# Performance work log

Hardware: AMD Instinct MI355X
Metric: run time of the kernel (lower is better)

The kernel has to match this reference:

```python
import jax, jax.numpy as jnp
import numpy as np

N_NODES = 50000
N_EDGES = 800000
IN_DIM = 128
OUT_DIM = 256


def setup_inputs() -> dict:
    key = jax.random.key(0)
    k1, k2, k3, k4 = jax.random.split(key, 4)
    feat = jax.random.normal(k1, (N_NODES, IN_DIM), dtype=jnp.float32)
    # xavier_uniform with relu gain, shape [in_dim, out_dim] (applied as h @ W)
    gain = np.sqrt(2.0)
    bound = gain * np.sqrt(6.0 / (IN_DIM + OUT_DIM))
    W = jax.random.uniform(k2, (IN_DIM, OUT_DIM), dtype=jnp.float32,
                           minval=-bound, maxval=bound)
    src = jax.random.randint(k3, (N_EDGES,), 0, N_NODES, dtype=jnp.int64)
    dst = jax.random.randint(k4, (N_EDGES,), 0, N_NODES, dtype=jnp.int64)
    return {"feat": feat, "W": W, "src": src, "dst": dst}


def reference(feat, W, src, dst):
    n = feat.shape[0]
    # mean aggregation over incoming neighbors (copy_src + mean on dst)
    msg_sum = jax.ops.segment_sum(feat[src], dst, num_segments=n)  # [N, in_dim]
    deg = jax.ops.segment_sum(jnp.ones_like(dst, dtype=feat.dtype), dst,
                              num_segments=n)  # [N]
    h_neigh = msg_sum / jnp.maximum(deg, 1.0)[:, None]  # zero-degree -> 0
    # self_loop=False path: fc((feat + h_neigh) / 2), then relu
    h = ((feat + h_neigh) * 0.5) @ W  # [N, out_dim]
    return jax.nn.relu(h)
```

## Files before the change

kernel.cpp:

```cpp
#include <hip/hip_runtime.h>
#include <hip/hip_fp16.h>

#define N_NODES 50000
#define N_EDGES 800000
#define IN_DIM  128
#define OUT_DIM 256
#define SCAN_BLOCKS ((N_NODES + 255) / 256)
#define WT_STRIDE 136

typedef _Float16 f16x8 __attribute__((ext_vector_type(8)));
typedef _Float16 f16x4 __attribute__((ext_vector_type(4)));
typedef float f32x4 __attribute__((ext_vector_type(4)));

__device__ __forceinline__ int detect_i64(const int* __restrict__ idx) {
  int orv = 0;
#pragma unroll
  for (int j = 1; j < 32; j += 2) orv |= idx[j];
  return orv == 0;
}

__global__ __launch_bounds__(256) void hist_cast(
    const int* __restrict__ dst, const float* __restrict__ feat,
    __half* __restrict__ feat16, int* __restrict__ hist,
    int* __restrict__ slot) {
  const int f = detect_i64(dst);
  const int e = blockIdx.x * 256 + threadIdx.x;
  const int d = dst[f ? 2 * (long)e : (long)e];
  slot[e] = atomicAdd(&hist[d], 1);

  if (feat16 != nullptr) {
    size_t i = (size_t)e * 8;
    float4 v0 = *reinterpret_cast<const float4*>(feat + i);
    float4 v1 = *reinterpret_cast<const float4*>(feat + i + 4);
    __half2 h[4];
    h[0] = __floats2half2_rn(v0.x, v0.y);
    h[1] = __floats2half2_rn(v0.z, v0.w);
    h[2] = __floats2half2_rn(v1.x, v1.y);
    h[3] = __floats2half2_rn(v1.z, v1.w);
    *reinterpret_cast<float4*>(feat16 + i) = *reinterpret_cast<float4*>(h);
  }
}

__global__ __launch_bounds__(256) void scan_block(
    const int* __restrict__ hist, int* __restrict__ row_start,
    int* __restrict__ bsum) {
  __shared__ int s[256];
  int tid = threadIdx.x;
  int i = blockIdx.x * 256 + tid;
  int v = (i < N_NODES) ? hist[i] : 0;
  s[tid] = v;
  __syncthreads();
  for (int off = 1; off < 256; off <<= 1) {
    int t = (tid >= off) ? s[tid - off] : 0;
    __syncthreads();
    s[tid] += t;
    __syncthreads();
  }
  if (i < N_NODES) row_start[i] = s[tid] - v;
  if (tid == 255) bsum[blockIdx.x] = s[255];
}

__global__ __launch_bounds__(256) void scan_add(
    const int* __restrict__ bsum, int* __restrict__ row_start) {
  __shared__ int sb[256];
  int tid = threadIdx.x;
  sb[tid] = (tid < (int)blockIdx.x) ? bsum[tid] : 0;
  __syncthreads();
  for (int off = 128; off > 0; off >>= 1) {
    if (tid < off) sb[tid] += sb[tid + off];
    __syncthreads();
  }
  int i = blockIdx.x * 256 + tid;
  if (i < N_NODES) row_start[i] += sb[0];
  if (i == 0) row_start[N_NODES] = N_EDGES;
}

__global__ __launch_bounds__(256) void scatter_kernel(
    const int* __restrict__ src, const int* __restrict__ dst,
    const int* __restrict__ row_start, const int* __restrict__ slot,
    int* __restrict__ esrc) {
  const int f = detect_i64(src);
  const int e = blockIdx.x * 256 + threadIdx.x;
  long off = f ? 2 * (long)e : (long)e;
  int d = dst[off];
  int s = src[off];
  esrc[row_start[d] + slot[e]] = s;
}

__global__ __launch_bounds__(256) void aggregate_f16(
    const float* __restrict__ feat, const __half* __restrict__ feat16,
    const int* __restrict__ esrc, const int* __restrict__ row_start,
    __half2* __restrict__ x) {
  int node = blockIdx.x * 4 + ((int)threadIdx.x >> 6);
  int lane = (int)threadIdx.x & 63;
  if (node >= N_NODES) return;
  int rs = row_start[node];
  int re = row_start[node + 1];
  float2 a0 = {0.f, 0.f}, a1 = {0.f, 0.f}, a2 = {0.f, 0.f}, a3 = {0.f, 0.f};
  int e = rs;
  for (; e + 3 < re; e += 4) {
    int s0 = esrc[e + 0];
    int s1 = esrc[e + 1];
    int s2 = esrc[e + 2];
    int s3 = esrc[e + 3];
    float2 v0 = __half22float2(*reinterpret_cast<const __half2*>(
        feat16 + (size_t)s0 * IN_DIM + lane * 2));
    float2 v1 = __half22float2(*reinterpret_cast<const __half2*>(
        feat16 + (size_t)s1 * IN_DIM + lane * 2));
    float2 v2 = __half22float2(*reinterpret_cast<const __half2*>(
        feat16 + (size_t)s2 * IN_DIM + lane * 2));
    float2 v3 = __half22float2(*reinterpret_cast<const __half2*>(
        feat16 + (size_t)s3 * IN_DIM + lane * 2));
    a0.x += v0.x; a0.y += v0.y;
    a1.x += v1.x; a1.y += v1.y;
    a2.x += v2.x; a2.y += v2.y;
    a3.x += v3.x; a3.y += v3.y;
  }
  for (; e < re; ++e) {
    float2 v0 = __half22float2(*reinterpret_cast<const __half2*>(
        feat16 + (size_t)esrc[e] * IN_DIM + lane * 2));
    a0.x += v0.x; a0.y += v0.y;
  }
  float deg = (float)(re - rs);
  float rdeg = (deg > 0.f) ? 1.0f / deg : 0.0f;
  float2 f = *reinterpret_cast<const float2*>(
      feat + (size_t)node * IN_DIM + lane * 2);
  float x0 = (f.x + (a0.x + a1.x + a2.x + a3.x) * rdeg) * 0.5f;
  float x1 = (f.y + (a0.y + a1.y + a2.y + a3.y) * rdeg) * 0.5f;
  x[(size_t)node * (IN_DIM / 2) + lane] = __floats2half2_rn(x0, x1);
}

__global__ __launch_bounds__(256) void aggregate_f32(
    const float* __restrict__ feat, const int* __restrict__ esrc,
    const int* __restrict__ row_start, __half2* __restrict__ x) {
  int node = blockIdx.x * 4 + ((int)threadIdx.x >> 6);
  int lane = (int)threadIdx.x & 63;
  if (node >= N_NODES) return;
  int rs = row_start[node];
  int re = row_start[node + 1];
  float2 a0 = {0.f, 0.f}, a1 = {0.f, 0.f};
  int e = rs;
  for (; e + 1 < re; e += 2) {
    float2 v0 = *reinterpret_cast<const float2*>(
        feat + (size_t)esrc[e] * IN_DIM + lane * 2);
    float2 v1 = *reinterpret_cast<const float2*>(
        feat + (size_t)esrc[e + 1] * IN_DIM + lane * 2);
    a0.x += v0.x; a0.y += v0.y;
    a1.x += v1.x; a1.y += v1.y;
  }
  if (e < re) {
    float2 v0 = *reinterpret_cast<const float2*>(
        feat + (size_t)esrc[e] * IN_DIM + lane * 2);
    a0.x += v0.x; a0.y += v0.y;
  }
  float deg = (float)(re - rs);
  float rdeg = (deg > 0.f) ? 1.0f / deg : 0.0f;
  float2 f = *reinterpret_cast<const float2*>(
      feat + (size_t)node * IN_DIM + lane * 2);
  float x0 = (f.x + (a0.x + a1.x) * rdeg) * 0.5f;
  float x1 = (f.y + (a0.y + a1.y) * rdeg) * 0.5f;
  x[(size_t)node * (IN_DIM / 2) + lane] = __floats2half2_rn(x0, x1);
}

__global__ __launch_bounds__(256) void mfma_gemm(
    const _Float16* __restrict__ x, const float* __restrict__ W,
    float* __restrict__ out) {
  __shared__ _Float16 WT[OUT_DIM * WT_STRIDE];

  const int tid = threadIdx.x;
  {
    const int n = tid;
#pragma unroll
    for (int k = 0; k < IN_DIM; k += 4) {
      f16x4 v;
      v.x = (_Float16)W[(k + 0) * OUT_DIM + n];
      v.y = (_Float16)W[(k + 1) * OUT_DIM + n];
      v.z = (_Float16)W[(k + 2) * OUT_DIM + n];
      v.w = (_Float16)W[(k + 3) * OUT_DIM + n];
      *reinterpret_cast<f16x4*>(&WT[n * WT_STRIDE + k]) = v;
    }
  }
  __syncthreads();

  const int wave = tid >> 6;
  const int lane = tid & 63;
  const int m = lane & 15;
  const int g = lane >> 4;
  const long row_base = (long)blockIdx.x * 128 + wave * 32;

  f16x8 a[2][4];
#pragma unroll
  for (int rt = 0; rt < 2; ++rt) {
    long row = row_base + rt * 16 + m;
#pragma unroll
    for (int kt = 0; kt < 4; ++kt) {
      if (row < N_NODES) {
        a[rt][kt] = *reinterpret_cast<const f16x8*>(
            x + row * IN_DIM + kt * 32 + g * 8);
      } else {
        a[rt][kt] = f16x8{};
      }
    }
  }

#pragma unroll
  for (int nt = 0; nt < 16; ++nt) {
    f16x8 b[4];
#pragma unroll
    for (int kt = 0; kt < 4; ++kt) {
      b[kt] = *reinterpret_cast<const f16x8*>(
          &WT[(nt * 16 + m) * WT_STRIDE + kt * 32 + g * 8]);
    }
    f32x4 acc0 = {0.f, 0.f, 0.f, 0.f};
    f32x4 acc1 = {0.f, 0.f, 0.f, 0.f};
#pragma unroll
    for (int kt = 0; kt < 4; ++kt) {
      acc0 = __builtin_amdgcn_mfma_f32_16x16x32_f16(a[0][kt], b[kt], acc0, 0, 0, 0);
      acc1 = __builtin_amdgcn_mfma_f32_16x16x32_f16(a[1][kt], b[kt], acc1, 0, 0, 0);
    }
    const int col = nt * 16 + m;
#pragma unroll
    for (int j = 0; j < 4; ++j) {
      long r0 = row_base + g * 4 + j;
      long r1 = row_base + 16 + g * 4 + j;
      if (r0 < N_NODES)
        __builtin_nontemporal_store(fmaxf(acc0[j], 0.f),
                                    &out[r0 * OUT_DIM + col]);
      if (r1 < N_NODES)
        __builtin_nontemporal_store(fmaxf(acc1[j], 0.f),
                                    &out[r1 * OUT_DIM + col]);
    }
  }
}

extern "C" void kernel_launch(void* const* d_in, const int* in_sizes, int n_in,
                              void* d_out, int out_size, void* d_ws,
                              size_t ws_size, hipStream_t stream) {
  const float* feat = (const float*)d_in[0];
  const float* W = (const float*)d_in[1];
  const int* src = (const int*)d_in[2];
  const int* dst = (const int*)d_in[3];
  float* out = (float*)d_out;

  char* p = (char*)d_ws;
  __half* x = (__half*)p;    p += (size_t)N_NODES * IN_DIM * 2;
  int* slot = (int*)x;
  int* esrc = (int*)p;       p += (size_t)N_EDGES * 4;
  int* hist = (int*)p;       p += (size_t)N_NODES * 4;
  int* row_start = (int*)p;  p += (size_t)(N_NODES + 1) * 4;
  int* bsum = (int*)p;       p += 256 * 4;
  p = (char*)(((uintptr_t)p + 15) & ~(uintptr_t)15);
  __half* feat16 = (__half*)p;
  size_t need_f16 =
      ((char*)feat16 - (char*)d_ws) + (size_t)N_NODES * IN_DIM * 2;
  const bool f16_path = (ws_size >= need_f16);

  hipMemsetAsync(hist, 0, (size_t)N_NODES * 4, stream);

  const int eblocks = N_EDGES / 256;
  hist_cast<<<eblocks, 256, 0, stream>>>(dst, feat,
                                         f16_path ? feat16 : nullptr, hist,
                                         slot);
  scan_block<<<SCAN_BLOCKS, 256, 0, stream>>>(hist, row_start, bsum);
  scan_add<<<SCAN_BLOCKS, 256, 0, stream>>>(bsum, row_start);
  scatter_kernel<<<eblocks, 256, 0, stream>>>(src, dst, row_start, slot, esrc);
  if (f16_path) {
    aggregate_f16<<<(N_NODES + 3) / 4, 256, 0, stream>>>(feat, feat16, esrc,
                                                         row_start,
                                                         (__half2*)x);
  } else {
    aggregate_f32<<<(N_NODES + 3) / 4, 256, 0, stream>>>(feat, esrc, row_start,
                                                         (__half2*)x);
  }
  mfma_gemm<<<(N_NODES + 127) / 128, 256, 0, stream>>>(
      (const _Float16*)x, W, out);
}
```

Before: 210.1 us.

## Pretranspose W once, vectorize scatter, unroll aggregation by 8, enlarge GEMM blocks

Transposes and casts W to fp16 once, inside the scan kernel, so each GEMM block fills shared memory with coalesced float4 copies instead of strided fp32 reads and conversions. The scatter kernel now handles two edges per thread with vector loads. The fp16 aggregation issues eight gathers per iteration with clamped indices, giving more memory-level parallelism. The GEMM moves to 512-thread blocks covering 256 rows, which halves how often W is staged, at the cost of lower occupancy from larger blocks.

```diff
diff --git a/kernel.cpp b/kernel.cpp
--- a/kernel.cpp
+++ b/kernel.cpp
@@ -9,7 +9,6 @@
 #define WT_STRIDE 136
 
 typedef _Float16 f16x8 __attribute__((ext_vector_type(8)));
-typedef _Float16 f16x4 __attribute__((ext_vector_type(4)));
 typedef float f32x4 __attribute__((ext_vector_type(4)));
 
 __device__ __forceinline__ int detect_i64(const int* __restrict__ idx) {
@@ -43,7 +42,8 @@
 
 __global__ __launch_bounds__(256) void scan_block(
     const int* __restrict__ hist, int* __restrict__ row_start,
-    int* __restrict__ bsum) {
+    int* __restrict__ bsum, const float* __restrict__ W,
+    __half* __restrict__ WT16g) {
   __shared__ int s[256];
   int tid = threadIdx.x;
   int i = blockIdx.x * 256 + tid;
@@ -58,6 +58,12 @@
   }
   if (i < N_NODES) row_start[i] = s[tid] - v;
   if (tid == 255) bsum[blockIdx.x] = s[255];
+
+  if (blockIdx.x < 128) {
+    int n = 2 * blockIdx.x + (tid >> 7);
+    int k = tid & 127;
+    WT16g[n * IN_DIM + k] = __float2half(W[k * OUT_DIM + n]);
+  }
 }
 
 __global__ __launch_bounds__(256) void scan_add(
@@ -80,11 +86,21 @@
     const int* __restrict__ row_start, const int* __restrict__ slot,
     int* __restrict__ esrc) {
   const int f = detect_i64(src);
-  const int e = blockIdx.x * 256 + threadIdx.x;
-  long off = f ? 2 * (long)e : (long)e;
-  int d = dst[off];
-  int s = src[off];
-  esrc[row_start[d] + slot[e]] = s;
+  const int t = blockIdx.x * 256 + threadIdx.x;
+  if (t >= N_EDGES / 2) return;
+  int s0, s1, d0, d1;
+  if (f) {
+    int4 sv = *reinterpret_cast<const int4*>(src + 4 * (long)t);
+    int4 dv = *reinterpret_cast<const int4*>(dst + 4 * (long)t);
+    s0 = sv.x; s1 = sv.z; d0 = dv.x; d1 = dv.z;
+  } else {
+    int2 sv = *reinterpret_cast<const int2*>(src + 2 * (long)t);
+    int2 dv = *reinterpret_cast<const int2*>(dst + 2 * (long)t);
+    s0 = sv.x; s1 = sv.y; d0 = dv.x; d1 = dv.y;
+  }
+  int2 sl = *reinterpret_cast<const int2*>(slot + 2 * (long)t);
+  esrc[row_start[d0] + sl.x] = s0;
+  esrc[row_start[d1] + sl.y] = s1;
 }
 
 __global__ __launch_bounds__(256) void aggregate_f16(
@@ -96,37 +112,35 @@
   if (node >= N_NODES) return;
   int rs = row_start[node];
   int re = row_start[node + 1];
-  float2 a0 = {0.f, 0.f}, a1 = {0.f, 0.f}, a2 = {0.f, 0.f}, a3 = {0.f, 0.f};
-  int e = rs;
-  for (; e + 3 < re; e += 4) {
-    int s0 = esrc[e + 0];
-    int s1 = esrc[e + 1];
-    int s2 = esrc[e + 2];
-    int s3 = esrc[e + 3];
-    float2 v0 = __half22float2(*reinterpret_cast<const __half2*>(
-        feat16 + (size_t)s0 * IN_DIM + lane * 2));
-    float2 v1 = __half22float2(*reinterpret_cast<const __half2*>(
-        feat16 + (size_t)s1 * IN_DIM + lane * 2));
-    float2 v2 = __half22float2(*reinterpret_cast<const __half2*>(
-        feat16 + (size_t)s2 * IN_DIM + lane * 2));
-    float2 v3 = __half22float2(*reinterpret_cast<const __half2*>(
-        feat16 + (size_t)s3 * IN_DIM + lane * 2));
-    a0.x += v0.x; a0.y += v0.y;
-    a1.x += v1.x; a1.y += v1.y;
-    a2.x += v2.x; a2.y += v2.y;
-    a3.x += v3.x; a3.y += v3.y;
-  }
-  for (; e < re; ++e) {
-    float2 v0 = __half22float2(*reinterpret_cast<const __half2*>(
-        feat16 + (size_t)esrc[e] * IN_DIM + lane * 2));
-    a0.x += v0.x; a0.y += v0.y;
-  }
+
+  float2 a[8];
+#pragma unroll
+  for (int j = 0; j < 8; ++j) a[j] = {0.f, 0.f};
+
+  for (int e = rs; e < re; e += 8) {
+    int idx[8];
+#pragma unroll
+    for (int j = 0; j < 8; ++j) idx[j] = esrc[min(e + j, re - 1)];
+#pragma unroll
+    for (int j = 0; j < 8; ++j) {
+      float2 v = __half22float2(*reinterpret_cast<const __half2*>(
+          feat16 + (size_t)idx[j] * IN_DIM + lane * 2));
+      if (e + j < re) {
+        a[j].x += v.x;
+        a[j].y += v.y;
+      }
+    }
+  }
+  float sx = ((a[0].x + a[1].x) + (a[2].x + a[3].x)) +
+             ((a[4].x + a[5].x) + (a[6].x + a[7].x));
+  float sy = ((a[0].y + a[1].y) + (a[2].y + a[3].y)) +
+             ((a[4].y + a[5].y) + (a[6].y + a[7].y));
   float deg = (float)(re - rs);
   float rdeg = (deg > 0.f) ? 1.0f / deg : 0.0f;
   float2 f = *reinterpret_cast<const float2*>(
       feat + (size_t)node * IN_DIM + lane * 2);
-  float x0 = (f.x + (a0.x + a1.x + a2.x + a3.x) * rdeg) * 0.5f;
-  float x1 = (f.y + (a0.y + a1.y + a2.y + a3.y) * rdeg) * 0.5f;
+  float x0 = (f.x + sx * rdeg) * 0.5f;
+  float x1 = (f.y + sy * rdeg) * 0.5f;
   x[(size_t)node * (IN_DIM / 2) + lane] = __floats2half2_rn(x0, x1);
 }
 
@@ -162,23 +176,19 @@
   x[(size_t)node * (IN_DIM / 2) + lane] = __floats2half2_rn(x0, x1);
 }
 
-__global__ __launch_bounds__(256) void mfma_gemm(
-    const _Float16* __restrict__ x, const float* __restrict__ W,
+__global__ __launch_bounds__(512) void mfma_gemm(
+    const _Float16* __restrict__ x, const __half* __restrict__ WT16g,
     float* __restrict__ out) {
   __shared__ _Float16 WT[OUT_DIM * WT_STRIDE];
 
   const int tid = threadIdx.x;
-  {
-    const int n = tid;
-#pragma unroll
-    for (int k = 0; k < IN_DIM; k += 4) {
-      f16x4 v;
-      v.x = (_Float16)W[(k + 0) * OUT_DIM + n];
-      v.y = (_Float16)W[(k + 1) * OUT_DIM + n];
-      v.z = (_Float16)W[(k + 2) * OUT_DIM + n];
-      v.w = (_Float16)W[(k + 3) * OUT_DIM + n];
-      *reinterpret_cast<f16x4*>(&WT[n * WT_STRIDE + k]) = v;
-    }
+#pragma unroll
+  for (int i = 0; i < 8; ++i) {
+    int c = i * 512 + tid;
+    int n = c >> 4;
+    int kc = c & 15;
+    *reinterpret_cast<float4*>(&WT[n * WT_STRIDE + kc * 8]) =
+        *reinterpret_cast<const float4*>(WT16g + c * 8);
   }
   __syncthreads();
 
@@ -186,7 +196,7 @@
   const int lane = tid & 63;
   const int m = lane & 15;
   const int g = lane >> 4;
-  const long row_base = (long)blockIdx.x * 128 + wave * 32;
+  const long row_base = (long)blockIdx.x * 256 + wave * 32;
 
   f16x8 a[2][4];
 #pragma unroll
@@ -250,6 +260,7 @@
   int* row_start = (int*)p;  p += (size_t)(N_NODES + 1) * 4;
   int* bsum = (int*)p;       p += 256 * 4;
   p = (char*)(((uintptr_t)p + 15) & ~(uintptr_t)15);
+  __half* WT16g = (__half*)p; p += (size_t)OUT_DIM * IN_DIM * 2;
   __half* feat16 = (__half*)p;
   size_t need_f16 =
       ((char*)feat16 - (char*)d_ws) + (size_t)N_NODES * IN_DIM * 2;
@@ -261,9 +272,10 @@
   hist_cast<<<eblocks, 256, 0, stream>>>(dst, feat,
                                          f16_path ? feat16 : nullptr, hist,
                                          slot);
-  scan_block<<<SCAN_BLOCKS, 256, 0, stream>>>(hist, row_start, bsum);
+  scan_block<<<SCAN_BLOCKS, 256, 0, stream>>>(hist, row_start, bsum, W, WT16g);
   scan_add<<<SCAN_BLOCKS, 256, 0, stream>>>(bsum, row_start);
-  scatter_kernel<<<eblocks, 256, 0, stream>>>(src, dst, row_start, slot, esrc);
+  scatter_kernel<<<(N_EDGES / 2 + 255) / 256, 256, 0, stream>>>(
+      src, dst, row_start, slot, esrc);
   if (f16_path) {
     aggregate_f16<<<(N_NODES + 3) / 4, 256, 0, stream>>>(feat, feat16, esrc,
                                                          row_start,
@@ -272,6 +284,6 @@
     aggregate_f32<<<(N_NODES + 3) / 4, 256, 0, stream>>>(feat, esrc, row_start,
                                                          (__half2*)x);
   }
-  mfma_gemm<<<(N_NODES + 127) / 128, 256, 0, stream>>>(
-      (const _Float16*)x, W, out);
-}
+  mfma_gemm<<<(N_NODES + 255) / 256, 512, 0, stream>>>(
+      (const _Float16*)x, WT16g, out);
+}
```

Measured after the change: 220.4 us. 4.9% more time.
